# Optimization experiments

Hardware: AMD Instinct MI355X
Metric: run time of the kernel (lower is better)

## Reference

```python
import jax, jax.numpy as jnp
import numpy as np

N_NODES = 100000
N_EDGES = 1600000
NFEAT = 512
HIDDEN = 128
NCLASS = 40


def setup_inputs() -> dict:
    key = jax.random.key(0)
    ks = jax.random.split(key, 8)
    x = jax.random.normal(ks[0], (N_NODES, NFEAT), dtype=jnp.float32)
    edge_src = jax.random.randint(ks[1], (N_EDGES,), 0, N_NODES, dtype=jnp.int32)
    edge_dst = jax.random.randint(ks[2], (N_EDGES,), 0, N_NODES, dtype=jnp.int32)
    # normalized adjacency values (D^-1/2 A D^-1/2 style), all positive
    edge_val = jax.random.uniform(ks[3], (N_EDGES,), dtype=jnp.float32)
    # glorot-ish init like pygcn's reset_parameters
    W1 = jax.random.normal(ks[4], (NFEAT, HIDDEN), dtype=jnp.float32) / np.sqrt(NFEAT)
    b1 = jnp.zeros((HIDDEN,), dtype=jnp.float32)
    W2 = jax.random.normal(ks[5], (HIDDEN, NCLASS), dtype=jnp.float32) / np.sqrt(HIDDEN)
    b2 = jnp.zeros((NCLASS,), dtype=jnp.float32)
    return {"x": x, "edge_src": edge_src, "edge_dst": edge_dst, "edge_val": edge_val,
            "W1": W1, "b1": b1, "W2": W2, "b2": b2}


def _gcn_layer(h, edge_src, edge_dst, edge_val, W, b):
    # support = h @ W ; out = spmm(adj, support) + b
    support = h @ W                                  # [N, d_out]
    msg = support[edge_src] * edge_val[:, None]      # [E, d_out] gather
    agg = jax.ops.segment_sum(msg, edge_dst, num_segments=N_NODES)  # scatter-add
    return agg + b


def reference(x, edge_src, edge_dst, edge_val, W1, b1, W2, b2):
    h = _gcn_layer(x, edge_src, edge_dst, edge_val, W1, b1)
    h = jax.nn.relu(h)
    # dropout=0.0 -> branch skipped (faithful to `if self.dropout:` with falsy value)
    h = _gcn_layer(h, edge_src, edge_dst, edge_val, W2, b2)
    return jax.nn.log_softmax(h, axis=1)
```

## Files before the change

### kernel.cpp

```cpp
#include <hip/hip_runtime.h>
#include <stdint.h>

#define NN 100000
#define NE 1600000
#define NF 512
#define NH 128
#define NC 40
#define DEGS 16
#define NGB 782
#define STRIPE 5
#define NEB 3125

typedef float f32x4 __attribute__((ext_vector_type(4)));
typedef short bf16x8 __attribute__((ext_vector_type(8)));

__device__ __forceinline__ unsigned short f2bf(float f){
    unsigned u = __float_as_uint(f);
    u = u + 0x7FFFu + ((u >> 16) & 1u);
    return (unsigned short)(u >> 16);
}
__device__ __forceinline__ unsigned pk2(float a, float b){
    return (unsigned)f2bf(a) | ((unsigned)f2bf(b) << 16);
}
__device__ __forceinline__ float blo(unsigned u){ return __uint_as_float(u << 16); }
__device__ __forceinline__ float bhi(unsigned u){ return __uint_as_float(u & 0xffff0000u); }
__device__ __forceinline__ float pval(unsigned p){ return __uint_as_float((p & 0x7fffu) << 16); }
__device__ __forceinline__ unsigned psrc(unsigned p){ return p >> 15; }

__global__ __launch_bounds__(256) void wprep(const float* __restrict__ W1, const float* __restrict__ W2,
                                             unsigned short* __restrict__ W1t, unsigned short* __restrict__ W2t){
    int tid = blockIdx.x * 256 + threadIdx.x;
    if (tid < NF * NH){
        int c = tid >> 9;
        int k = tid & 511;
        W1t[c * NF + k] = f2bf(W1[k * NH + c]);
    }
    int t2 = tid - NF * NH;
    if (t2 >= 0 && t2 < 48 * NH){
        int c = t2 >> 7;
        int k = t2 & 127;
        W2t[c * NH + k] = (c < NC) ? f2bf(W2[k * NC + c]) : (unsigned short)0;
    }
}

__global__ __launch_bounds__(256, 3) void gemm1_edge(const float* __restrict__ x,
                                                     const unsigned short* __restrict__ W1t,
                                                     unsigned short* __restrict__ s1,
                                                     const int* __restrict__ esrc,
                                                     const int* __restrict__ edst,
                                                     const float* __restrict__ eval,
                                                     unsigned* __restrict__ deg,
                                                     unsigned* __restrict__ pkc){
    __shared__ unsigned short Al[2][128 * 40];
    __shared__ unsigned short Bl[2][128 * 40];
    const int bid = blockIdx.x;
    const int tid = threadIdx.x;

    if (bid % STRIPE != 0){
        int ebid = (bid / STRIPE) * 4 + (bid % STRIPE) - 1;
        int t0 = ebid * 512 + tid;
#pragma unroll
        for (int i = 0; i < 2; i++){
            int e = t0 + i * 256;
            if (e < NE){
                int d = edst[e];
                unsigned pv = ((unsigned)esrc[e] << 15) | ((unsigned)f2bf(eval[e]) & 0x7fffu);
                unsigned pos = atomicAdd(&deg[d * DEGS], 1u);
                if (pos < 64u)
                    pkc[(size_t)d * 64 + pos] = pv;
            }
        }
        return;
    }

    const int wid  = tid >> 6;
    const int lane = tid & 63;
    const int quad = lane >> 4;
    const int l15  = lane & 15;
    const int br   = (bid / STRIPE) * 128;

    const int r    = tid >> 1;
    const int half = tid & 1;

    int arow = br + r; if (arow >= NN) arow = NN - 1;
    const float* aptr = x + (size_t)arow * NF + half * 16;
    const unsigned short* bptr = W1t + (size_t)r * NF + half * 16;

    float4 pa0, pa1, pa2, pa3;
    uint4  pb0, pb1;
    {
        const float4* ap = (const float4*)aptr;
        pa0 = ap[0]; pa1 = ap[1]; pa2 = ap[2]; pa3 = ap[3];
        const uint4* bp = (const uint4*)bptr;
        pb0 = bp[0]; pb1 = bp[1];
        unsigned* Ad = (unsigned*)&Al[0][r * 40 + half * 16];
        Ad[0] = pk2(pa0.x, pa0.y); Ad[1] = pk2(pa0.z, pa0.w);
        Ad[2] = pk2(pa1.x, pa1.y); Ad[3] = pk2(pa1.z, pa1.w);
        Ad[4] = pk2(pa2.x, pa2.y); Ad[5] = pk2(pa2.z, pa2.w);
        Ad[6] = pk2(pa3.x, pa3.y); Ad[7] = pk2(pa3.z, pa3.w);
        uint4* Bd = (uint4*)&Bl[0][r * 40 + half * 16];
        Bd[0] = pb0; Bd[1] = pb1;
    }
    __syncthreads();

    f32x4 acc[2][8];
#pragma unroll
    for (int i = 0; i < 2; i++)
#pragma unroll
        for (int j = 0; j < 8; j++) acc[i][j] = (f32x4){0.f, 0.f, 0.f, 0.f};

    int cur = 0;
    for (int ks = 0; ks < NF; ks += 32){
        const bool more = (ks + 32 < NF);
        if (more){
            const float4* ap = (const float4*)(aptr + ks + 32);
            pa0 = ap[0]; pa1 = ap[1]; pa2 = ap[2]; pa3 = ap[3];
            const uint4* bp = (const uint4*)(bptr + ks + 32);
            pb0 = bp[0]; pb1 = bp[1];
        }

        bf16x8 a0 = *(const bf16x8*)&Al[cur][(wid * 32 +      l15) * 40 + quad * 8];
        bf16x8 a1 = *(const bf16x8*)&Al[cur][(wid * 32 + 16 + l15) * 40 + quad * 8];
        bf16x8 bb[8];
#pragma unroll
        for (int ct = 0; ct < 8; ct++)
            bb[ct] = *(const bf16x8*)&Bl[cur][(ct * 16 + l15) * 40 + quad * 8];
#pragma unroll
        for (int ct = 0; ct < 8; ct++){
            acc[0][ct] = __builtin_amdgcn_mfma_f32_16x16x32_bf16(a0, bb[ct], acc[0][ct], 0, 0, 0);
            acc[1][ct] = __builtin_amdgcn_mfma_f32_16x16x32_bf16(a1, bb[ct], acc[1][ct], 0, 0, 0);
        }

        if (more){
            int nxt = cur ^ 1;
            unsigned* Ad = (unsigned*)&Al[nxt][r * 40 + half * 16];
            Ad[0] = pk2(pa0.x, pa0.y); Ad[1] = pk2(pa0.z, pa0.w);
            Ad[2] = pk2(pa1.x, pa1.y); Ad[3] = pk2(pa1.z, pa1.w);
            Ad[4] = pk2(pa2.x, pa2.y); Ad[5] = pk2(pa2.z, pa2.w);
            Ad[6] = pk2(pa3.x, pa3.y); Ad[7] = pk2(pa3.z, pa3.w);
            uint4* Bd = (uint4*)&Bl[nxt][r * 40 + half * 16];
            Bd[0] = pb0; Bd[1] = pb1;
        }
        __syncthreads();
        cur ^= 1;
    }

#pragma unroll
    for (int rt = 0; rt < 2; rt++)
#pragma unroll
        for (int ct = 0; ct < 8; ct++)
#pragma unroll
            for (int i = 0; i < 4; i++){
                int row = br + wid * 32 + rt * 16 + quad * 4 + i;
                if (row < NN) s1[(size_t)row * NH + ct * 16 + l15] = f2bf(acc[rt][ct][i]);
            }
}

__global__ __launch_bounds__(256) void agg1g2(const uint4* __restrict__ s1v,
                                              const unsigned* __restrict__ deg,
                                              const unsigned* __restrict__ pkc,
                                              const float* __restrict__ b1,
                                              const unsigned short* __restrict__ W2t,
                                              unsigned short* __restrict__ s2p){
    __shared__ unsigned short Hl[64][136];
    const int tid   = threadIdx.x;
    const int wid   = tid >> 6;
    const int lane  = tid & 63;
    const int quad  = lane >> 4;
    const int hl    = lane & 15;
    const int lbase = quad * 16;
    const int nb    = blockIdx.x * 64;

    const float4* b1v = (const float4*)b1;
    const float4 bA = b1v[2 * hl], bB = b1v[2 * hl + 1];

#pragma unroll
    for (int pass = 0; pass < 4; pass++){
        const int nloc = pass * 16 + wid * 4 + quad;
        const int node = nb + nloc;
        float a[8];
#pragma unroll
        for (int t = 0; t < 8; t++) a[t] = 0.f;

        if (node < NN){
            const unsigned s = (unsigned)node * 64;
            unsigned dgv = deg[node * DEGS]; int dg = (dgv > 64u) ? 64 : (int)dgv;
            const unsigned e = s + dg;

            unsigned rec = 0;
            { int c0 = dg > 16 ? 16 : dg; if (hl < c0) rec = pkc[s + hl]; }
            for (unsigned base = s; base < e; base += 16){
                int cnt = (int)(e - base); if (cnt > 16) cnt = 16;
                unsigned curc = rec;
                unsigned nxb = base + 16;
                if (nxb < e){
                    int cn = (int)(e - nxb); if (cn > 16) cn = 16;
                    rec = 0;
                    if (hl < cn) rec = pkc[nxb + hl];
                }
                int j = 0;
                for (; j + 8 <= cnt; j += 8){
                    unsigned ps[8];
#pragma unroll
                    for (int q = 0; q < 8; q++) ps[q] = __shfl(curc, lbase + j + q, 64);
                    uint4 us[8];
#pragma unroll
                    for (int q = 0; q < 8; q++) us[q] = s1v[(size_t)psrc(ps[q]) * 16 + hl];
#pragma unroll
                    for (int q = 0; q < 8; q++){
                        float v = pval(ps[q]);
                        a[0] += v * blo(us[q].x); a[1] += v * bhi(us[q].x);
                        a[2] += v * blo(us[q].y); a[3] += v * bhi(us[q].y);
                        a[4] += v * blo(us[q].z); a[5] += v * bhi(us[q].z);
                        a[6] += v * blo(us[q].w); a[7] += v * bhi(us[q].w);
                    }
                }
                for (; j < cnt; j++){
                    unsigned p = __shfl(curc, lbase + j, 64);
                    float v = pval(p);
                    uint4 u  = s1v[(size_t)psrc(p) * 16 + hl];
                    a[0] += v * blo(u.x); a[1] += v * bhi(u.x);
                    a[2] += v * blo(u.y); a[3] += v * bhi(u.y);
                    a[4] += v * blo(u.z); a[5] += v * bhi(u.z);
                    a[6] += v * blo(u.w); a[7] += v * bhi(u.w);
                }
            }
            a[0] += bA.x; a[1] += bA.y; a[2] += bA.z; a[3] += bA.w;
            a[4] += bB.x; a[5] += bB.y; a[6] += bB.z; a[7] += bB.w;
#pragma unroll
            for (int t = 0; t < 8; t++) a[t] = fmaxf(a[t], 0.f);
        }
        *(uint4*)&Hl[nloc][hl * 8] = make_uint4(pk2(a[0], a[1]), pk2(a[2], a[3]),
                                                pk2(a[4], a[5]), pk2(a[6], a[7]));
    }
    __syncthreads();

    bf16x8 bf[3][4];
#pragma unroll
    for (int ct = 0; ct < 3; ct++)
#pragma unroll
        for (int ks = 0; ks < 4; ks++)
            bf[ct][ks] = *(const bf16x8*)&W2t[(ct * 16 + hl) * NH + ks * 32 + quad * 8];

    bf16x8 af[4];
#pragma unroll
    for (int ks = 0; ks < 4; ks++)
        af[ks] = *(const bf16x8*)&Hl[wid * 16 + hl][ks * 32 + quad * 8];

    f32x4 acc[3];
#pragma unroll
    for (int ct = 0; ct < 3; ct++) acc[ct] = (f32x4){0.f, 0.f, 0.f, 0.f};
#pragma unroll
    for (int ks = 0; ks < 4; ks++)
#pragma unroll
        for (int ct = 0; ct < 3; ct++)
            acc[ct] = __builtin_amdgcn_mfma_f32_16x16x32_bf16(af[ks], bf[ct][ks], acc[ct], 0, 0, 0);

#pragma unroll
    for (int ct = 0; ct < 3; ct++)
#pragma unroll
        for (int i = 0; i < 4; i++){
            int row = nb + wid * 16 + quad * 4 + i;
            if (row < NN) s2p[(size_t)row * 64 + ct * 16 + hl] = f2bf(acc[ct][i]);
        }
}

__global__ __launch_bounds__(256) void agg2(const uint4* __restrict__ s2v,
                                            const unsigned* __restrict__ deg,
                                            const unsigned* __restrict__ pkc,
                                            const float* __restrict__ b2, float* __restrict__ out){
    const int lane  = threadIdx.x & 63;
    const int oct   = lane >> 3;
    const int hl    = lane & 7;
    const int lbase = oct * 8;
    const int node  = blockIdx.x * 32 + (threadIdx.x >> 6) * 8 + oct;

    float a[8];
#pragma unroll
    for (int t = 0; t < 8; t++) a[t] = 0.f;

    const unsigned s = (unsigned)node * 64;
    unsigned dgv = deg[node * DEGS]; int dg = (dgv > 64u) ? 64 : (int)dgv;
    const unsigned e = s + dg;

    unsigned rec = 0;
    { int c0 = dg > 8 ? 8 : dg; if (hl < c0) rec = pkc[s + hl]; }
    for (unsigned base = s; base < e; base += 8){
        int cnt = (int)(e - base); if (cnt > 8) cnt = 8;
        unsigned curc = rec;
        unsigned nxb = base + 8;
        if (nxb < e){
            int cn = (int)(e - nxb); if (cn > 8) cn = 8;
            rec = 0;
            if (hl < cn) rec = pkc[nxb + hl];
        }
        int j = 0;
        for (; j + 4 <= cnt; j += 4){
            unsigned ps[4];
#pragma unroll
            for (int q = 0; q < 4; q++) ps[q] = __shfl(curc, lbase + j + q, 64);
            uint4 us[4];
#pragma unroll
            for (int q = 0; q < 4; q++) us[q] = s2v[(size_t)psrc(ps[q]) * 8 + hl];
#pragma unroll
            for (int q = 0; q < 4; q++){
                float v = pval(ps[q]);
                a[0] += v * blo(us[q].x); a[1] += v * bhi(us[q].x);
                a[2] += v * blo(us[q].y); a[3] += v * bhi(us[q].y);
                a[4] += v * blo(us[q].z); a[5] += v * bhi(us[q].z);
                a[6] += v * blo(us[q].w); a[7] += v * bhi(us[q].w);
            }
        }
        for (; j < cnt; j++){
            unsigned p = __shfl(curc, lbase + j, 64);
            float v = pval(p);
            uint4 u  = s2v[(size_t)psrc(p) * 8 + hl];
            a[0] += v * blo(u.x); a[1] += v * bhi(u.x);
            a[2] += v * blo(u.y); a[3] += v * bhi(u.y);
            a[4] += v * blo(u.z); a[5] += v * bhi(u.z);
            a[6] += v * blo(u.w); a[7] += v * bhi(u.w);
        }
    }
    const bool act = hl < 5;
    float z[8];
    if (act){
        const float4* b2v = (const float4*)b2;
        float4 cA = b2v[2 * hl], cB = b2v[2 * hl + 1];
        z[0] = a[0] + cA.x; z[1] = a[1] + cA.y; z[2] = a[2] + cA.z; z[3] = a[3] + cA.w;
        z[4] = a[4] + cB.x; z[5] = a[5] + cB.y; z[6] = a[6] + cB.z; z[7] = a[7] + cB.w;
    } else {
#pragma unroll
        for (int t = 0; t < 8; t++) z[t] = -INFINITY;
    }
    float m = z[0];
#pragma unroll
    for (int t = 1; t < 8; t++) m = fmaxf(m, z[t]);
#pragma unroll
    for (int o = 4; o; o >>= 1) m = fmaxf(m, __shfl_xor(m, o, 64));
    float pe = 0.f;
    if (act){
#pragma unroll
        for (int t = 0; t < 8; t++) pe += __expf(z[t] - m);
    }
#pragma unroll
    for (int o = 4; o; o >>= 1) pe += __shfl_xor(pe, o, 64);
    if (act){
        float l = __logf(pe) + m;
        float* op = out + (size_t)node * NC + 8 * hl;
        *(float4*)op       = make_float4(z[0] - l, z[1] - l, z[2] - l, z[3] - l);
        *(float4*)(op + 4) = make_float4(z[4] - l, z[5] - l, z[6] - l, z[7] - l);
    }
}

extern "C" void kernel_launch(void* const* d_in, const int* in_sizes, int n_in,
                              void* d_out, int out_size, void* d_ws, size_t ws_size,
                              hipStream_t stream) {
    const float* x    = (const float*)d_in[0];
    const int*   esrc = (const int*)  d_in[1];
    const int*   edst = (const int*)  d_in[2];
    const float* eval = (const float*)d_in[3];
    const float* W1   = (const float*)d_in[4];
    const float* b1   = (const float*)d_in[5];
    const float* W2   = (const float*)d_in[6];
    const float* b2   = (const float*)d_in[7];
    float* out = (float*)d_out;

    char* ws = (char*)d_ws;
    size_t off = 0;
    auto alloc = [&](size_t bytes) -> void* {
        void* p = ws + off;
        off += (bytes + 255) & ~(size_t)255;
        return p;
    };
    unsigned short* W1t  = (unsigned short*)alloc((size_t)NF * NH * 2);
    unsigned short* W2t  = (unsigned short*)alloc((size_t)48 * NH * 2);
    unsigned short* s1   = (unsigned short*)alloc((size_t)NN * NH * 2);
    unsigned short* s2p  = (unsigned short*)alloc((size_t)NN * 64 * 2);
    unsigned*       deg  = (unsigned*)     alloc((size_t)NN * DEGS * 4);
    unsigned*       pkc  = (unsigned*)     alloc((size_t)NN * 64 * 4);

    hipMemsetAsync(deg, 0, (size_t)NN * DEGS * 4, stream);

    wprep     <<<280, 256, 0, stream>>>(W1, W2, W1t, W2t);
    gemm1_edge<<<NGB * STRIPE, 256, 0, stream>>>(x, W1t, s1, esrc, edst, eval, deg, pkc);
    agg1g2    <<<(NN + 63) / 64, 256, 0, stream>>>((const uint4*)s1, deg, pkc, b1, W2t, s2p);
    agg2      <<<NN / 32, 256, 0, stream>>>((const uint4*)s2p, deg, pkc, b2, out);
}
```

Before: 489.9 us.

## Partition gather by source-node range passes to improve cache locality

Both aggregation kernels now load all of a node's packed edge records up front. They then sweep over source-node ranges of 8192 rows (NPASS passes), and in each pass gather only the edges whose source falls in the current range, using ballot and ffs loops. The aim is to keep concurrently running waves hitting the same slice of the support matrix so it stays in L2 or the MALL. In exchange, the 8-wide batched loads that exposed memory-level parallelism become serialized one-at-a-time gathers, and each wave pays about 13 passes of ballot overhead.

```diff
diff --git a/kernel.cpp b/kernel.cpp
--- a/kernel.cpp
+++ b/kernel.cpp
@@ -9,7 +9,8 @@
 #define DEGS 16
 #define NGB 782
 #define STRIPE 5
-#define NEB 3125
+#define RSH 13
+#define NPASS ((NN + (1 << RSH) - 1) >> RSH)
 
 typedef float f32x4 __attribute__((ext_vector_type(4)));
 typedef short bf16x8 __attribute__((ext_vector_type(8)));
@@ -174,7 +175,6 @@
     const float4* b1v = (const float4*)b1;
     const float4 bA = b1v[2 * hl], bB = b1v[2 * hl + 1];
 
-#pragma unroll
     for (int pass = 0; pass < 4; pass++){
         const int nloc = pass * 16 + wid * 4 + quad;
         const int node = nb + nloc;
@@ -182,49 +182,41 @@
 #pragma unroll
         for (int t = 0; t < 8; t++) a[t] = 0.f;
 
+        unsigned rec[4]; rec[0] = 0; rec[1] = 0; rec[2] = 0; rec[3] = 0;
+        int dg = 0;
         if (node < NN){
+            unsigned dgv = deg[node * DEGS]; dg = (dgv > 64u) ? 64 : (int)dgv;
             const unsigned s = (unsigned)node * 64;
-            unsigned dgv = deg[node * DEGS]; int dg = (dgv > 64u) ? 64 : (int)dgv;
-            const unsigned e = s + dg;
-
-            unsigned rec = 0;
-            { int c0 = dg > 16 ? 16 : dg; if (hl < c0) rec = pkc[s + hl]; }
-            for (unsigned base = s; base < e; base += 16){
-                int cnt = (int)(e - base); if (cnt > 16) cnt = 16;
-                unsigned curc = rec;
-                unsigned nxb = base + 16;
-                if (nxb < e){
-                    int cn = (int)(e - nxb); if (cn > 16) cn = 16;
-                    rec = 0;
-                    if (hl < cn) rec = pkc[nxb + hl];
-                }
-                int j = 0;
-                for (; j + 8 <= cnt; j += 8){
-                    unsigned ps[8];
-#pragma unroll
-                    for (int q = 0; q < 8; q++) ps[q] = __shfl(curc, lbase + j + q, 64);
-                    uint4 us[8];
-#pragma unroll
-                    for (int q = 0; q < 8; q++) us[q] = s1v[(size_t)psrc(ps[q]) * 16 + hl];
-#pragma unroll
-                    for (int q = 0; q < 8; q++){
-                        float v = pval(ps[q]);
-                        a[0] += v * blo(us[q].x); a[1] += v * bhi(us[q].x);
-                        a[2] += v * blo(us[q].y); a[3] += v * bhi(us[q].y);
-                        a[4] += v * blo(us[q].z); a[5] += v * bhi(us[q].z);
-                        a[6] += v * blo(us[q].w); a[7] += v * bhi(us[q].w);
+            if (dg >  0) rec[0] = pkc[s      + hl];
+            if (dg > 16) rec[1] = pkc[s + 16 + hl];
+            if (dg > 32) rec[2] = pkc[s + 32 + hl];
+            if (dg > 48) rec[3] = pkc[s + 48 + hl];
+        }
+        int wmax = dg;
+        wmax = max(wmax, __shfl_xor(wmax, 16, 64));
+        wmax = max(wmax, __shfl_xor(wmax, 32, 64));
+
+        for (int p = 0; p < NPASS; p++){
+#pragma unroll
+            for (int c = 0; c < 4; c++){
+                if ((c << 4) < wmax){
+                    bool mine = (hl < dg - (c << 4)) && ((int)(psrc(rec[c]) >> RSH) == p);
+                    unsigned long long bal = __ballot(mine);
+                    unsigned m = (unsigned)(bal >> lbase) & 0xFFFFu;
+                    while (m){
+                        int b = __ffs(m) - 1; m &= m - 1;
+                        unsigned pcr = __shfl(rec[c], lbase + b, 64);
+                        float v = pval(pcr);
+                        uint4 u = s1v[(size_t)psrc(pcr) * 16 + hl];
+                        a[0] += v * blo(u.x); a[1] += v * bhi(u.x);
+                        a[2] += v * blo(u.y); a[3] += v * bhi(u.y);
+                        a[4] += v * blo(u.z); a[5] += v * bhi(u.z);
+                        a[6] += v * blo(u.w); a[7] += v * bhi(u.w);
                     }
                 }
-                for (; j < cnt; j++){
-                    unsigned p = __shfl(curc, lbase + j, 64);
-                    float v = pval(p);
-                    uint4 u  = s1v[(size_t)psrc(p) * 16 + hl];
-                    a[0] += v * blo(u.x); a[1] += v * bhi(u.x);
-                    a[2] += v * blo(u.y); a[3] += v * bhi(u.y);
-                    a[4] += v * blo(u.z); a[5] += v * bhi(u.z);
-                    a[6] += v * blo(u.w); a[7] += v * bhi(u.w);
-                }
             }
+        }
+        if (node < NN){
             a[0] += bA.x; a[1] += bA.y; a[2] += bA.z; a[3] += bA.w;
             a[4] += bB.x; a[5] += bB.y; a[6] += bB.z; a[7] += bB.w;
 #pragma unroll
@@ -279,46 +271,38 @@
 #pragma unroll
     for (int t = 0; t < 8; t++) a[t] = 0.f;
 
+    unsigned rec[8];
+#pragma unroll
+    for (int c = 0; c < 8; c++) rec[c] = 0;
     const unsigned s = (unsigned)node * 64;
     unsigned dgv = deg[node * DEGS]; int dg = (dgv > 64u) ? 64 : (int)dgv;
-    const unsigned e = s + dg;
-
-    unsigned rec = 0;
-    { int c0 = dg > 8 ? 8 : dg; if (hl < c0) rec = pkc[s + hl]; }
-    for (unsigned base = s; base < e; base += 8){
-        int cnt = (int)(e - base); if (cnt > 8) cnt = 8;
-        unsigned curc = rec;
-        unsigned nxb = base + 8;
-        if (nxb < e){
-            int cn = (int)(e - nxb); if (cn > 8) cn = 8;
-            rec = 0;
-            if (hl < cn) rec = pkc[nxb + hl];
-        }
-        int j = 0;
-        for (; j + 4 <= cnt; j += 4){
-            unsigned ps[4];
-#pragma unroll
-            for (int q = 0; q < 4; q++) ps[q] = __shfl(curc, lbase + j + q, 64);
-            uint4 us[4];
-#pragma unroll
-            for (int q = 0; q < 4; q++) us[q] = s2v[(size_t)psrc(ps[q]) * 8 + hl];
-#pragma unroll
-            for (int q = 0; q < 4; q++){
-                float v = pval(ps[q]);
-                a[0] += v * blo(us[q].x); a[1] += v * bhi(us[q].x);
-                a[2] += v * blo(us[q].y); a[3] += v * bhi(us[q].y);
-                a[4] += v * blo(us[q].z); a[5] += v * bhi(us[q].z);
-                a[6] += v * blo(us[q].w); a[7] += v * bhi(us[q].w);
+#pragma unroll
+    for (int c = 0; c < 8; c++)
+        if (dg > (c << 3)) rec[c] = pkc[s + (c << 3) + hl];
+
+    int wmax = dg;
+    wmax = max(wmax, __shfl_xor(wmax, 8, 64));
+    wmax = max(wmax, __shfl_xor(wmax, 16, 64));
+    wmax = max(wmax, __shfl_xor(wmax, 32, 64));
+
+    for (int p = 0; p < NPASS; p++){
+#pragma unroll
+        for (int c = 0; c < 8; c++){
+            if ((c << 3) < wmax){
+                bool mine = (hl < dg - (c << 3)) && ((int)(psrc(rec[c]) >> RSH) == p);
+                unsigned long long bal = __ballot(mine);
+                unsigned m = (unsigned)(bal >> lbase) & 0xFFu;
+                while (m){
+                    int b = __ffs(m) - 1; m &= m - 1;
+                    unsigned pcr = __shfl(rec[c], lbase + b, 64);
+                    float v = pval(pcr);
+                    uint4 u = s2v[(size_t)psrc(pcr) * 8 + hl];
+                    a[0] += v * blo(u.x); a[1] += v * bhi(u.x);
+                    a[2] += v * blo(u.y); a[3] += v * bhi(u.y);
+                    a[4] += v * blo(u.z); a[5] += v * bhi(u.z);
+                    a[6] += v * blo(u.w); a[7] += v * bhi(u.w);
+                }
             }
-        }
-        for (; j < cnt; j++){
-            unsigned p = __shfl(curc, lbase + j, 64);
-            float v = pval(p);
-            uint4 u  = s2v[(size_t)psrc(p) * 8 + hl];
-            a[0] += v * blo(u.x); a[1] += v * bhi(u.x);
-            a[2] += v * blo(u.y); a[3] += v * bhi(u.y);
-            a[4] += v * blo(u.z); a[5] += v * bhi(u.z);
-            a[6] += v * blo(u.w); a[7] += v * bhi(u.w);
         }
     }
     const bool act = hl < 5;
```

Result: slower. 520.8 us (+6.3%).
